# Kernel optimization log

Measured on AMD Instinct MI355X. Metric: run time of the kernel, lower is better.

Reference implementation:

```python
import jax, jax.numpy as jnp
import numpy as np

NUM_HEADS = 16
HIDDEN = 1024
HEAD_DIM = HIDDEN // NUM_HEADS
B, L = 1, 2048


def setup_inputs() -> dict:
    key = jax.random.key(0)
    ks = jax.random.split(key, 5)
    scale = 1.0 / np.sqrt(HIDDEN)
    x = jax.random.normal(ks[0], (B, L, HIDDEN), dtype=jnp.float32)
    Wq = jax.random.normal(ks[1], (HIDDEN, HIDDEN), dtype=jnp.float32) * scale
    Wk = jax.random.normal(ks[2], (HIDDEN, HIDDEN), dtype=jnp.float32) * scale
    Wv = jax.random.normal(ks[3], (HIDDEN, HIDDEN), dtype=jnp.float32) * scale
    Wo = jax.random.normal(ks[4], (HIDDEN, HIDDEN), dtype=jnp.float32) * scale
    return {"x": x, "Wq": Wq, "Wk": Wk, "Wv": Wv, "Wo": Wo}


def reference(x, Wq, Wk, Wv, Wo):
    Bx, Lx, _ = x.shape
    # nn.Linear computes x @ W.T (bias=False)
    q = (x @ Wq.T).reshape(Bx, Lx, NUM_HEADS, HEAD_DIM)
    k = (x @ Wk.T).reshape(Bx, Lx, NUM_HEADS, HEAD_DIM)
    v = (x @ Wv.T).reshape(Bx, Lx, NUM_HEADS, HEAD_DIM)
    # elu(.)+1 feature map
    q = jax.nn.elu(q) + 1.0
    k = jax.nn.elu(k) + 1.0
    # causal linear-attention state via cumsum of kv outer products
    kv = jnp.einsum('blhd,blhe->blhde', k, v)           # [B,L,H,D,D]
    kv_cumsum = jnp.cumsum(kv, axis=1)
    k_cumsum = jnp.cumsum(k, axis=1)
    out = jnp.einsum('blhd,blhde->blhe', q, kv_cumsum)   # [B,L,H,D]
    denom = jnp.clip(jnp.einsum('blhd,blhd->blh', q, k_cumsum), 1e-6, None)
    out = out / denom[..., None]
    return out.reshape(Bx, Lx, HIDDEN) @ Wo.T
```

## Files before the change

kernel.cpp:

```cpp
#include <hip/hip_runtime.h>
#include <hip/hip_bf16.h>

typedef __attribute__((ext_vector_type(8))) short short8;
typedef __attribute__((ext_vector_type(4))) float floatx4;
typedef __attribute__((ext_vector_type(8))) unsigned short ushortx8;
typedef __attribute__((ext_vector_type(4))) unsigned short ushortx4;
typedef unsigned short u16;

#define HIDDEN 1024
#define NH 16
#define HD 64
#define SEQ 2048
#define CHUNK 128
#define NCHUNK (SEQ / CHUNK)

__device__ __forceinline__ u16 f2bf(float f) {
    union { float f; unsigned u; } v; v.f = f;
    unsigned r = v.u + 0x7fffu + ((v.u >> 16) & 1u);
    return (u16)(r >> 16);
}
__device__ __forceinline__ float bf2f(u16 u) {
    union { unsigned u; float f; } v; v.u = ((unsigned)u) << 16;
    return v.f;
}

__device__ __forceinline__ void gl_lds16(const u16* g, u16* l) {
    __builtin_amdgcn_global_load_lds(
        (const __attribute__((address_space(1))) void*)g,
        (__attribute__((address_space(3))) void*)l,
        16, 0, 0);
}

__global__ __launch_bounds__(256)
void convert_all(const float* __restrict__ x,  const float* __restrict__ Wq,
                 const float* __restrict__ Wk, const float* __restrict__ Wv,
                 const float* __restrict__ Wo,
                 u16* __restrict__ xb, u16* __restrict__ Wb, u16* __restrict__ Wob)
{
    const int total4 = 1572864;
    for (int idx = blockIdx.x * 256 + threadIdx.x; idx < total4; idx += gridDim.x * 256) {
        const float4* src; u16* dst; int off;
        if (idx < 524288)       { src = (const float4*)x;  dst = xb;            off = idx; }
        else if (idx < 786432)  { src = (const float4*)Wq; dst = Wb;            off = idx - 524288; }
        else if (idx < 1048576) { src = (const float4*)Wk; dst = Wb + 1048576;  off = idx - 786432; }
        else if (idx < 1310720) { src = (const float4*)Wv; dst = Wb + 2097152;  off = idx - 1048576; }
        else                    { src = (const float4*)Wo; dst = Wob;           off = idx - 1310720; }
        float4 v = src[off];
        ushortx4 u = { f2bf(v.x), f2bf(v.y), f2bf(v.z), f2bf(v.w) };
        *(ushortx4*)(dst + (size_t)off * 4) = u;
    }
}

template<int TM, bool ELU, typename OutT>
__global__ __launch_bounds__(256, 2)
void gemm_m97(const u16* __restrict__ A, const u16* __restrict__ Bm,
              OutT* __restrict__ C, const int K, const int ldc)
{
    constexpr int FI = TM / 32;
    __shared__ u16 As[TM * 64];
    __shared__ u16 Bs[128 * 64];
    const int m0 = blockIdx.y * TM, n0 = blockIdx.x * 128;
    const int t = threadIdx.x;
    const int lane = t & 63, wave = t >> 6;
    const int ln = lane & 15, q4 = lane >> 4;
    const int wm = (wave >> 1) * (TM / 2);
    const int wn = (wave & 1) * 64;
    const int r_in = t >> 3;
    const int csw = (((t & 7) ^ (r_in & 7)) << 3);

    const u16* Ag = A + (size_t)(m0 + r_in) * K + csw;
    const u16* Bg = Bm + (size_t)(n0 + r_in) * K + csw;

    floatx4 acc[FI][4];
#pragma unroll
    for (int i = 0; i < FI; i++)
#pragma unroll
        for (int j = 0; j < 4; j++) acc[i][j] = (floatx4)0.0f;

    for (int k0 = 0; k0 < K; k0 += 64) {
        if (k0) __syncthreads();
#pragma unroll
        for (int i = 0; i < FI; i++)
            gl_lds16(Ag + (size_t)i * 32 * K, &As[i * 2048 + t * 8]);
#pragma unroll
        for (int i = 0; i < 4; i++)
            gl_lds16(Bg + (size_t)i * 32 * K, &Bs[i * 2048 + t * 8]);
        Ag += 64; Bg += 64;
        __syncthreads();
#pragma unroll
        for (int s = 0; s < 2; s++) {
            const int rc = (((s * 4 + q4) ^ (ln & 7)) << 3);
            short8 af[FI], bfr[4];
#pragma unroll
            for (int i = 0; i < FI; i++)
                af[i] = *(const short8*)&As[(wm + i * 16 + ln) * 64 + rc];
#pragma unroll
            for (int j = 0; j < 4; j++)
                bfr[j] = *(const short8*)&Bs[(wn + j * 16 + ln) * 64 + rc];
#pragma unroll
            for (int i = 0; i < FI; i++)
#pragma unroll
                for (int j = 0; j < 4; j++)
                    acc[i][j] = __builtin_amdgcn_mfma_f32_16x16x32_bf16(af[i], bfr[j], acc[i][j], 0, 0, 0);
        }
    }
#pragma unroll
    for (int i = 0; i < FI; i++)
#pragma unroll
        for (int j = 0; j < 4; j++)
#pragma unroll
            for (int rr = 0; rr < 4; rr++) {
                int m = m0 + wm + i * 16 + q4 * 4 + rr;
                int n = n0 + wn + j * 16 + ln;
                float v = acc[i][j][rr];
                if (ELU && n < 2048) v = (v > 0.f) ? (v + 1.f) : __expf(v);
                if constexpr (sizeof(OutT) == 2) C[(size_t)m * ldc + n] = f2bf(v);
                else                             C[(size_t)m * ldc + n] = v;
            }
}

__global__ __launch_bounds__(256, 2)
void chunk_stats(const u16* __restrict__ qkv,
                 float* __restrict__ S_ws, float* __restrict__ ksum_ws)
{
    __shared__ u16 kT[64 * 136];
    __shared__ u16 vT[64 * 136];
    const int c = blockIdx.x, h = blockIdx.y;
    const int t = threadIdx.x;
    const int lane = t & 63, wave = t >> 6;
    const int ln = lane & 15, q4 = lane >> 4;
    {
        const int row = t >> 1, sc = (t & 1) * 32;
        const size_t gk = (size_t)(c * CHUNK + row) * 3072 + 1024 + h * HD + sc;
        u16 kr[32], vr[32];
#pragma unroll
        for (int i = 0; i < 4; i++) {
            *(ushortx8*)&kr[i * 8] = *(const ushortx8*)(qkv + gk + i * 8);
            *(ushortx8*)&vr[i * 8] = *(const ushortx8*)(qkv + gk + 1024 + i * 8);
        }
#pragma unroll
        for (int j = 0; j < 32; j++) {
            kT[(sc + j) * 136 + row] = kr[j];
            vT[(sc + j) * 136 + row] = vr[j];
        }
    }
    __syncthreads();
    floatx4 sacc[4];
#pragma unroll
    for (int j = 0; j < 4; j++) sacc[j] = (floatx4)0.0f;
#pragma unroll
    for (int ks = 0; ks < 4; ks++) {
        short8 af = *(const short8*)&kT[(wave * 16 + ln) * 136 + ks * 32 + q4 * 8];
#pragma unroll
        for (int j = 0; j < 4; j++) {
            short8 bfr = *(const short8*)&vT[(j * 16 + ln) * 136 + ks * 32 + q4 * 8];
            sacc[j] = __builtin_amdgcn_mfma_f32_16x16x32_bf16(af, bfr, sacc[j], 0, 0, 0);
        }
    }
    float* Sp = S_ws + ((size_t)(h * NCHUNK + c) << 12);
#pragma unroll
    for (int j = 0; j < 4; j++)
#pragma unroll
        for (int r = 0; r < 4; r++) {
            int d = wave * 16 + q4 * 4 + r;
            int e = j * 16 + ln;
            Sp[e * 64 + d] = sacc[j][r];
        }
    if (t < 64) {
        float s = 0.f;
#pragma unroll
        for (int j = 0; j < 128; j++) s += bf2f(kT[t * 136 + j]);
        ksum_ws[(h * NCHUNK + c) * 64 + t] = s;
    }
}

__global__ __launch_bounds__(256, 1)
void attn_out(const u16* __restrict__ qkv, const float* __restrict__ S_ws,
              const float* __restrict__ ksum_ws, u16* __restrict__ attnb)
{
    __shared__ __align__(16) u16 smem[32384];
    u16* q_l   = smem;
    u16* k_l   = smem + 9216;
    u16* P_l   = smem;
    u16* vT_l  = smem + 18432;
    u16* kvT_l = smem + 27136;
    float* kpref  = (float*)(smem + 31744);
    float* denom2 = kpref + 64;

    const int c = blockIdx.x, h = blockIdx.y;
    const int t = threadIdx.x;
    const int lane = t & 63, wave = t >> 6;
    const int ln = lane & 15, q4 = lane >> 4;

    {
        const int row = t >> 1, sc = (t & 1) * 32;
        const size_t gq = (size_t)(c * CHUNK + row) * 3072 + h * HD + sc;
#pragma unroll
        for (int i = 0; i < 4; i++) {
            *(ushortx8*)&q_l[row * 72 + sc + i * 8] = *(const ushortx8*)(qkv + gq + i * 8);
            *(ushortx8*)&k_l[row * 72 + sc + i * 8] = *(const ushortx8*)(qkv + gq + 1024 + i * 8);
        }
        u16 vr[32];
#pragma unroll
        for (int i = 0; i < 4; i++) *(ushortx8*)&vr[i * 8] = *(const ushortx8*)(qkv + gq + 2048 + i * 8);
#pragma unroll
        for (int j = 0; j < 32; j++) vT_l[(sc + j) * 136 + row] = vr[j];
    }
    {
        const int e = t >> 2, db = (t & 3) * 16;
        float kv[16];
#pragma unroll
        for (int i = 0; i < 16; i++) kv[i] = 0.f;
        for (int cp = 0; cp < c; cp++) {
            const float* Sp = S_ws + ((size_t)(h * NCHUNK + cp) << 12) + e * 64 + db;
#pragma unroll
            for (int g = 0; g < 4; g++) {
                float4 s4 = *(const float4*)(Sp + g * 4);
                kv[g * 4 + 0] += s4.x; kv[g * 4 + 1] += s4.y;
                kv[g * 4 + 2] += s4.z; kv[g * 4 + 3] += s4.w;
            }
        }
#pragma unroll
        for (int g = 0; g < 4; g++) {
            ushortx4 u = { f2bf(kv[g * 4 + 0]), f2bf(kv[g * 4 + 1]),
                           f2bf(kv[g * 4 + 2]), f2bf(kv[g * 4 + 3]) };
            *(ushortx4*)&kvT_l[e * 72 + db + g * 4] = u;
        }
        if (t < 64) {
            float s = 0.f;
            for (int cp = 0; cp < c; cp++) s += ksum_ws[(h * NCHUNK + cp) * 64 + t];
            kpref[t] = s;
        }
    }
    __syncthreads();

    const int pm = (wave >> 1) * 64, pn = (wave & 1) * 64;
    floatx4 pacc[4][4];
#pragma unroll
    for (int i = 0; i < 4; i++)
#pragma unroll
        for (int j = 0; j < 4; j++) pacc[i][j] = (floatx4)0.0f;
#pragma unroll
    for (int s = 0; s < 2; s++) {
        short8 af[4], bfr[4];
#pragma unroll
        for (int i = 0; i < 4; i++)
            af[i] = *(const short8*)&q_l[(pm + i * 16 + ln) * 72 + s * 32 + q4 * 8];
#pragma unroll
        for (int j = 0; j < 4; j++)
            bfr[j] = *(const short8*)&k_l[(pn + j * 16 + ln) * 72 + s * 32 + q4 * 8];
#pragma unroll
        for (int i = 0; i < 4; i++)
#pragma unroll
            for (int j = 0; j < 4; j++)
                pacc[i][j] = __builtin_amdgcn_mfma_f32_16x16x32_bf16(af[i], bfr[j], pacc[i][j], 0, 0, 0);
    }
#pragma unroll
    for (int i = 0; i < 4; i++)
#pragma unroll
        for (int r = 0; r < 4; r++) {
            int rowi = pm + i * 16 + q4 * 4 + r;
            float rs = 0.f;
#pragma unroll
            for (int j = 0; j < 4; j++) {
                int col = pn + j * 16 + ln;
                float p = pacc[i][j][r];
                if (col > rowi) p = 0.f;
                pacc[i][j][r] = p;
                rs += p;
            }
#pragma unroll
            for (int off = 1; off < 16; off <<= 1) rs += __shfl_xor(rs, off, 64);
            if (ln == 0) denom2[(wave & 1) * 128 + rowi] = rs;
        }
    const int ob = wave * 32;
    floatx4 oacc[2][4];
#pragma unroll
    for (int i = 0; i < 2; i++)
#pragma unroll
        for (int j = 0; j < 4; j++) oacc[i][j] = (floatx4)0.0f;
#pragma unroll
    for (int s = 0; s < 2; s++) {
        short8 af[2], bfr[4];
#pragma unroll
        for (int i2 = 0; i2 < 2; i2++)
            af[i2] = *(const short8*)&q_l[(ob + i2 * 16 + ln) * 72 + s * 32 + q4 * 8];
#pragma unroll
        for (int j = 0; j < 4; j++)
            bfr[j] = *(const short8*)&kvT_l[(j * 16 + ln) * 72 + s * 32 + q4 * 8];
#pragma unroll
        for (int i2 = 0; i2 < 2; i2++)
#pragma unroll
            for (int j = 0; j < 4; j++)
                oacc[i2][j] = __builtin_amdgcn_mfma_f32_16x16x32_bf16(af[i2], bfr[j], oacc[i2][j], 0, 0, 0);
    }
    __syncthreads();
    if (t < 128) {
        float s = 0.f;
#pragma unroll
        for (int d = 0; d < 64; d++) s += bf2f(q_l[t * 72 + d]) * kpref[d];
        denom2[t] += s;
    }
    __syncthreads();
#pragma unroll
    for (int i = 0; i < 4; i++)
#pragma unroll
        for (int j = 0; j < 4; j++)
#pragma unroll
            for (int r = 0; r < 4; r++) {
                int rowi = pm + i * 16 + q4 * 4 + r;
                int col = pn + j * 16 + ln;
                P_l[rowi * 136 + col] = f2bf(pacc[i][j][r]);
            }
    __syncthreads();
    for (int ks = 0; ks <= wave; ks++) {
        short8 af[2], bfr[4];
#pragma unroll
        for (int i2 = 0; i2 < 2; i2++)
            af[i2] = *(const short8*)&P_l[(ob + i2 * 16 + ln) * 136 + ks * 32 + q4 * 8];
#pragma unroll
        for (int j = 0; j < 4; j++)
            bfr[j] = *(const short8*)&vT_l[(j * 16 + ln) * 136 + ks * 32 + q4 * 8];
#pragma unroll
        for (int i2 = 0; i2 < 2; i2++)
#pragma unroll
            for (int j = 0; j < 4; j++)
                oacc[i2][j] = __builtin_amdgcn_mfma_f32_16x16x32_bf16(af[i2], bfr[j], oacc[i2][j], 0, 0, 0);
    }
#pragma unroll
    for (int i2 = 0; i2 < 2; i2++)
#pragma unroll
        for (int j = 0; j < 4; j++)
#pragma unroll
            for (int r = 0; r < 4; r++) {
                int rowi = ob + i2 * 16 + q4 * 4 + r;
                int e = j * 16 + ln;
                float den = denom2[rowi] + denom2[128 + rowi];
                den = fmaxf(den, 1e-6f);
                float val = oacc[i2][j][r] / den;
                attnb[(size_t)(c * CHUNK + rowi) * HIDDEN + h * HD + e] = f2bf(val);
            }
}

extern "C" void kernel_launch(void* const* d_in, const int* in_sizes, int n_in,
                              void* d_out, int out_size, void* d_ws, size_t ws_size,
                              hipStream_t stream)
{
    const float* x  = (const float*)d_in[0];
    const float* Wq = (const float*)d_in[1];
    const float* Wk = (const float*)d_in[2];
    const float* Wv = (const float*)d_in[3];
    const float* Wo = (const float*)d_in[4];
    float* out = (float*)d_out;

    char* ws = (char*)d_ws;
    const size_t MB = 1024 * 1024;
    u16* qkvb  = (u16*)(ws);
    u16* xb    = (u16*)(ws + 12 * MB);
    u16* attnb = (u16*)(ws + 12 * MB);
    u16* Wb    = (u16*)(ws + 16 * MB);
    float* S_ws    = (float*)(ws + 16 * MB);
    float* ksum_ws = (float*)(ws + 20 * MB);
    u16* Wob   = (u16*)(ws + 22 * MB);

    convert_all<<<2048, 256, 0, stream>>>(x, Wq, Wk, Wv, Wo, xb, Wb, Wob);
    gemm_m97<128, true, u16><<<dim3(24, 16), 256, 0, stream>>>(xb, Wb, qkvb, 1024, 3072);
    chunk_stats<<<dim3(NCHUNK, NH), 256, 0, stream>>>(qkvb, S_ws, ksum_ws);
    attn_out<<<dim3(NCHUNK, NH), 256, 0, stream>>>(qkvb, S_ws, ksum_ws, attnb);
    gemm_m97<64, false, float><<<dim3(8, 32), 256, 0, stream>>>(attnb, Wob, out, 1024, 1024);
}
```

Before: 137.5 us.

## Emit transposed K/V from QKV GEMM and shrink GEMM tiles for occupancy

The QKV GEMM epilogue now writes Q/K row-major plus K and V transposed per head, so the chunk_stats and attn_out kernels can load with direct global-to-LDS copies into swizzled layouts. This replaces the scalar LDS transposes. Both GEMMs move to 64-row tiles with more blocks and higher launch bounds to fill more CUs. The cost is extra global writes for the transposed copies and scattered 8-byte stores in the epilogue.

```diff
diff --git a/kernel.cpp b/kernel.cpp
--- a/kernel.cpp
+++ b/kernel.cpp
@@ -51,98 +51,102 @@
     }
 }
 
-template<int TM, bool ELU, typename OutT>
-__global__ __launch_bounds__(256, 2)
-void gemm_m97(const u16* __restrict__ A, const u16* __restrict__ Bm,
-              OutT* __restrict__ C, const int K, const int ldc)
-{
-    constexpr int FI = TM / 32;
-    __shared__ u16 As[TM * 64];
+__global__ __launch_bounds__(256, 3)
+void qkv_gemm64(const u16* __restrict__ A, const u16* __restrict__ Bm,
+                u16* __restrict__ qkb, u16* __restrict__ kT_b, u16* __restrict__ vT_b)
+{
+    __shared__ u16 As[64 * 64];
     __shared__ u16 Bs[128 * 64];
-    const int m0 = blockIdx.y * TM, n0 = blockIdx.x * 128;
+    const int n0 = blockIdx.x * 128, m0 = blockIdx.y * 64;
     const int t = threadIdx.x;
     const int lane = t & 63, wave = t >> 6;
     const int ln = lane & 15, q4 = lane >> 4;
-    const int wm = (wave >> 1) * (TM / 2);
-    const int wn = (wave & 1) * 64;
+    const int wm = (wave >> 1) * 32, wn = (wave & 1) * 64;
     const int r_in = t >> 3;
     const int csw = (((t & 7) ^ (r_in & 7)) << 3);
 
-    const u16* Ag = A + (size_t)(m0 + r_in) * K + csw;
-    const u16* Bg = Bm + (size_t)(n0 + r_in) * K + csw;
-
-    floatx4 acc[FI][4];
-#pragma unroll
-    for (int i = 0; i < FI; i++)
+    const u16* Ag = A + (size_t)(m0 + r_in) * 1024 + csw;
+    const u16* Bg = Bm + (size_t)(n0 + r_in) * 1024 + csw;
+
+    floatx4 acc[2][4];
+#pragma unroll
+    for (int i = 0; i < 2; i++)
 #pragma unroll
         for (int j = 0; j < 4; j++) acc[i][j] = (floatx4)0.0f;
 
-    for (int k0 = 0; k0 < K; k0 += 64) {
+    for (int k0 = 0; k0 < 1024; k0 += 64) {
         if (k0) __syncthreads();
-#pragma unroll
-        for (int i = 0; i < FI; i++)
-            gl_lds16(Ag + (size_t)i * 32 * K, &As[i * 2048 + t * 8]);
+        gl_lds16(Ag, &As[t * 8]);
+        gl_lds16(Ag + 32 * 1024, &As[2048 + t * 8]);
 #pragma unroll
         for (int i = 0; i < 4; i++)
-            gl_lds16(Bg + (size_t)i * 32 * K, &Bs[i * 2048 + t * 8]);
+            gl_lds16(Bg + (size_t)i * 32 * 1024, &Bs[i * 2048 + t * 8]);
         Ag += 64; Bg += 64;
         __syncthreads();
 #pragma unroll
         for (int s = 0; s < 2; s++) {
             const int rc = (((s * 4 + q4) ^ (ln & 7)) << 3);
-            short8 af[FI], bfr[4];
-#pragma unroll
-            for (int i = 0; i < FI; i++)
+            short8 af[2], bfr[4];
+#pragma unroll
+            for (int i = 0; i < 2; i++)
                 af[i] = *(const short8*)&As[(wm + i * 16 + ln) * 64 + rc];
 #pragma unroll
             for (int j = 0; j < 4; j++)
                 bfr[j] = *(const short8*)&Bs[(wn + j * 16 + ln) * 64 + rc];
 #pragma unroll
-            for (int i = 0; i < FI; i++)
+            for (int i = 0; i < 2; i++)
 #pragma unroll
                 for (int j = 0; j < 4; j++)
                     acc[i][j] = __builtin_amdgcn_mfma_f32_16x16x32_bf16(af[i], bfr[j], acc[i][j], 0, 0, 0);
         }
     }
-#pragma unroll
-    for (int i = 0; i < FI; i++)
-#pragma unroll
-        for (int j = 0; j < 4; j++)
-#pragma unroll
-            for (int rr = 0; rr < 4; rr++) {
-                int m = m0 + wm + i * 16 + q4 * 4 + rr;
-                int n = n0 + wn + j * 16 + ln;
-                float v = acc[i][j][rr];
-                if (ELU && n < 2048) v = (v > 0.f) ? (v + 1.f) : __expf(v);
-                if constexpr (sizeof(OutT) == 2) C[(size_t)m * ldc + n] = f2bf(v);
-                else                             C[(size_t)m * ldc + n] = v;
-            }
+    const int grp = n0 >> 10;
+#pragma unroll
+    for (int i = 0; i < 2; i++)
+#pragma unroll
+        for (int j = 0; j < 4; j++) {
+            const int mb = m0 + wm + i * 16 + q4 * 4;
+            const int n = n0 + wn + j * 16 + ln;
+            const int nh = n & 1023, h = nh >> 6, e = nh & 63;
+            float vals[4];
+#pragma unroll
+            for (int r = 0; r < 4; r++) {
+                float v = acc[i][j][r];
+                if (grp < 2) v = (v > 0.f) ? (v + 1.f) : __expf(v);
+                vals[r] = v;
+            }
+            if (grp == 0) {
+#pragma unroll
+                for (int r = 0; r < 4; r++) qkb[(size_t)(mb + r) * 2048 + nh] = f2bf(vals[r]);
+            } else if (grp == 1) {
+#pragma unroll
+                for (int r = 0; r < 4; r++) qkb[(size_t)(mb + r) * 2048 + 1024 + nh] = f2bf(vals[r]);
+                ushortx4 u = { f2bf(vals[0]), f2bf(vals[1]), f2bf(vals[2]), f2bf(vals[3]) };
+                *(ushortx4*)&kT_b[(size_t)(h * 64 + e) * 2048 + mb] = u;
+            } else {
+                ushortx4 u = { f2bf(vals[0]), f2bf(vals[1]), f2bf(vals[2]), f2bf(vals[3]) };
+                *(ushortx4*)&vT_b[(size_t)(h * 64 + e) * 2048 + mb] = u;
+            }
+        }
 }
 
 __global__ __launch_bounds__(256, 2)
-void chunk_stats(const u16* __restrict__ qkv,
-                 float* __restrict__ S_ws, float* __restrict__ ksum_ws)
-{
-    __shared__ u16 kT[64 * 136];
-    __shared__ u16 vT[64 * 136];
+void chunk_stats2(const u16* __restrict__ kT_b, const u16* __restrict__ vT_b,
+                  float* __restrict__ S_ws, float* __restrict__ ksum_ws)
+{
+    __shared__ u16 kT_l[64 * 128];
+    __shared__ u16 vT_l[64 * 128];
     const int c = blockIdx.x, h = blockIdx.y;
     const int t = threadIdx.x;
-    const int lane = t & 63, wave = t >> 6;
+    const int lane = t & 63, w = t >> 6;
     const int ln = lane & 15, q4 = lane >> 4;
-    {
-        const int row = t >> 1, sc = (t & 1) * 32;
-        const size_t gk = (size_t)(c * CHUNK + row) * 3072 + 1024 + h * HD + sc;
-        u16 kr[32], vr[32];
-#pragma unroll
-        for (int i = 0; i < 4; i++) {
-            *(ushortx8*)&kr[i * 8] = *(const ushortx8*)(qkv + gk + i * 8);
-            *(ushortx8*)&vr[i * 8] = *(const ushortx8*)(qkv + gk + 1024 + i * 8);
-        }
-#pragma unroll
-        for (int j = 0; j < 32; j++) {
-            kT[(sc + j) * 136 + row] = kr[j];
-            vT[(sc + j) * 136 + row] = vr[j];
-        }
+#pragma unroll
+    for (int i = 0; i < 4; i++) {
+        const int d0 = w * 16 + i * 4 + (lane >> 4);
+        const int cc = lane & 15;
+        const size_t gsrc = (size_t)(h * 64 + d0) * 2048 + c * 128 + ((cc ^ (d0 & 7)) << 3);
+        gl_lds16(kT_b + gsrc, &kT_l[(w * 16 + i * 4) * 128 + lane * 8]);
+        gl_lds16(vT_b + gsrc, &vT_l[(w * 16 + i * 4) * 128 + lane * 8]);
     }
     __syncthreads();
     floatx4 sacc[4];
@@ -150,10 +154,11 @@
     for (int j = 0; j < 4; j++) sacc[j] = (floatx4)0.0f;
 #pragma unroll
     for (int ks = 0; ks < 4; ks++) {
-        short8 af = *(const short8*)&kT[(wave * 16 + ln) * 136 + ks * 32 + q4 * 8];
+        const int rc = (((ks * 4 + q4) ^ (ln & 7)) << 3);
+        short8 af = *(const short8*)&kT_l[(w * 16 + ln) * 128 + rc];
 #pragma unroll
         for (int j = 0; j < 4; j++) {
-            short8 bfr = *(const short8*)&vT[(j * 16 + ln) * 136 + ks * 32 + q4 * 8];
+            short8 bfr = *(const short8*)&vT_l[(j * 16 + ln) * 128 + rc];
             sacc[j] = __builtin_amdgcn_mfma_f32_16x16x32_bf16(af, bfr, sacc[j], 0, 0, 0);
         }
     }
@@ -162,49 +167,52 @@
     for (int j = 0; j < 4; j++)
 #pragma unroll
         for (int r = 0; r < 4; r++) {
-            int d = wave * 16 + q4 * 4 + r;
+            int d = w * 16 + q4 * 4 + r;
             int e = j * 16 + ln;
             Sp[e * 64 + d] = sacc[j][r];
         }
     if (t < 64) {
         float s = 0.f;
 #pragma unroll
-        for (int j = 0; j < 128; j++) s += bf2f(kT[t * 136 + j]);
+        for (int cc = 0; cc < 16; cc++) {
+            ushortx8 v8 = *(const ushortx8*)&kT_l[t * 128 + cc * 8];
+#pragma unroll
+            for (int jj = 0; jj < 8; jj++) s += bf2f(v8[jj]);
+        }
         ksum_ws[(h * NCHUNK + c) * 64 + t] = s;
     }
 }
 
 __global__ __launch_bounds__(256, 1)
-void attn_out(const u16* __restrict__ qkv, const float* __restrict__ S_ws,
-              const float* __restrict__ ksum_ws, u16* __restrict__ attnb)
-{
-    __shared__ __align__(16) u16 smem[32384];
+void attn_out2(const u16* __restrict__ qkb, const u16* __restrict__ vT_b,
+               const float* __restrict__ S_ws, const float* __restrict__ ksum_ws,
+               u16* __restrict__ attnb)
+{
+    __shared__ __align__(16) u16 smem[29824];
     u16* q_l   = smem;
-    u16* k_l   = smem + 9216;
+    u16* k_l   = smem + 8192;
+    u16* kvT_l = smem + 16384;
     u16* P_l   = smem;
-    u16* vT_l  = smem + 18432;
-    u16* kvT_l = smem + 27136;
-    float* kpref  = (float*)(smem + 31744);
+    u16* vT_l  = smem + 20992;
+    float* kpref  = (float*)(smem + 29184);
     float* denom2 = kpref + 64;
 
     const int c = blockIdx.x, h = blockIdx.y;
     const int t = threadIdx.x;
-    const int lane = t & 63, wave = t >> 6;
+    const int lane = t & 63, w = t >> 6;
     const int ln = lane & 15, q4 = lane >> 4;
 
-    {
-        const int row = t >> 1, sc = (t & 1) * 32;
-        const size_t gq = (size_t)(c * CHUNK + row) * 3072 + h * HD + sc;
-#pragma unroll
-        for (int i = 0; i < 4; i++) {
-            *(ushortx8*)&q_l[row * 72 + sc + i * 8] = *(const ushortx8*)(qkv + gq + i * 8);
-            *(ushortx8*)&k_l[row * 72 + sc + i * 8] = *(const ushortx8*)(qkv + gq + 1024 + i * 8);
-        }
-        u16 vr[32];
-#pragma unroll
-        for (int i = 0; i < 4; i++) *(ushortx8*)&vr[i * 8] = *(const ushortx8*)(qkv + gq + 2048 + i * 8);
-#pragma unroll
-        for (int j = 0; j < 32; j++) vT_l[(sc + j) * 136 + row] = vr[j];
+#pragma unroll
+    for (int i = 0; i < 4; i++) {
+        const int l = i * 32 + w * 8 + (lane >> 3);
+        const int cc = lane & 7;
+        const size_t gq = (size_t)(c * CHUNK + l) * 2048 + h * 64 + ((cc ^ (l & 7)) << 3);
+        gl_lds16(qkb + gq,        &q_l[(i * 32 + w * 8) * 64 + lane * 8]);
+        gl_lds16(qkb + gq + 1024, &k_l[(i * 32 + w * 8) * 64 + lane * 8]);
+        const int d0 = w * 16 + i * 4 + (lane >> 4);
+        const int cv = lane & 15;
+        gl_lds16(vT_b + (size_t)(h * 64 + d0) * 2048 + c * 128 + ((cv ^ (d0 & 7)) << 3),
+                 &vT_l[(w * 16 + i * 4) * 128 + lane * 8]);
     }
     {
         const int e = t >> 2, db = (t & 3) * 16;
@@ -234,7 +242,7 @@
     }
     __syncthreads();
 
-    const int pm = (wave >> 1) * 64, pn = (wave & 1) * 64;
+    const int pm = (w >> 1) * 64, pn = (w & 1) * 64;
     floatx4 pacc[4][4];
 #pragma unroll
     for (int i = 0; i < 4; i++)
@@ -242,13 +250,14 @@
         for (int j = 0; j < 4; j++) pacc[i][j] = (floatx4)0.0f;
 #pragma unroll
     for (int s = 0; s < 2; s++) {
+        const int rc = (((s * 4 + q4) ^ (ln & 7)) << 3);
         short8 af[4], bfr[4];
 #pragma unroll
         for (int i = 0; i < 4; i++)
-            af[i] = *(const short8*)&q_l[(pm + i * 16 + ln) * 72 + s * 32 + q4 * 8];
+            af[i] = *(const short8*)&q_l[(pm + i * 16 + ln) * 64 + rc];
 #pragma unroll
         for (int j = 0; j < 4; j++)
-            bfr[j] = *(const short8*)&k_l[(pn + j * 16 + ln) * 72 + s * 32 + q4 * 8];
+            bfr[j] = *(const short8*)&k_l[(pn + j * 16 + ln) * 64 + rc];
 #pragma unroll
         for (int i = 0; i < 4; i++)
 #pragma unroll
@@ -271,9 +280,9 @@
             }
 #pragma unroll
             for (int off = 1; off < 16; off <<= 1) rs += __shfl_xor(rs, off, 64);
-            if (ln == 0) denom2[(wave & 1) * 128 + rowi] = rs;
-        }
-    const int ob = wave * 32;
+            if (ln == 0) denom2[(w & 1) * 128 + rowi] = rs;
+        }
+    const int ob = w * 32;
     floatx4 oacc[2][4];
 #pragma unroll
     for (int i = 0; i < 2; i++)
@@ -281,10 +290,11 @@
         for (int j = 0; j < 4; j++) oacc[i][j] = (floatx4)0.0f;
 #pragma unroll
     for (int s = 0; s < 2; s++) {
+        const int rc = (((s * 4 + q4) ^ (ln & 7)) << 3);
         short8 af[2], bfr[4];
 #pragma unroll
         for (int i2 = 0; i2 < 2; i2++)
-            af[i2] = *(const short8*)&q_l[(ob + i2 * 16 + ln) * 72 + s * 32 + q4 * 8];
+            af[i2] = *(const short8*)&q_l[(ob + i2 * 16 + ln) * 64 + rc];
 #pragma unroll
         for (int j = 0; j < 4; j++)
             bfr[j] = *(const short8*)&kvT_l[(j * 16 + ln) * 72 + s * 32 + q4 * 8];
@@ -298,7 +308,11 @@
     if (t < 128) {
         float s = 0.f;
 #pragma unroll
-        for (int d = 0; d < 64; d++) s += bf2f(q_l[t * 72 + d]) * kpref[d];
+        for (int c8 = 0; c8 < 8; c8++) {
+            ushortx8 v8 = *(const ushortx8*)&q_l[t * 64 + ((c8 ^ (t & 7)) << 3)];
+#pragma unroll
+            for (int jj = 0; jj < 8; jj++) s += bf2f(v8[jj]) * kpref[c8 * 8 + jj];
+        }
         denom2[t] += s;
     }
     __syncthreads();
@@ -313,14 +327,15 @@
                 P_l[rowi * 136 + col] = f2bf(pacc[i][j][r]);
             }
     __syncthreads();
-    for (int ks = 0; ks <= wave; ks++) {
+    for (int ks = 0; ks <= w; ks++) {
         short8 af[2], bfr[4];
 #pragma unroll
         for (int i2 = 0; i2 < 2; i2++)
             af[i2] = *(const short8*)&P_l[(ob + i2 * 16 + ln) * 136 + ks * 32 + q4 * 8];
+        const int rc = (((ks * 4 + q4) ^ (ln & 7)) << 3);
 #pragma unroll
         for (int j = 0; j < 4; j++)
-            bfr[j] = *(const short8*)&vT_l[(j * 16 + ln) * 136 + ks * 32 + q4 * 8];
+            bfr[j] = *(const short8*)&vT_l[(j * 16 + ln) * 128 + rc];
 #pragma unroll
         for (int i2 = 0; i2 < 2; i2++)
 #pragma unroll
@@ -342,6 +357,66 @@
             }
 }
 
+__global__ __launch_bounds__(256, 3)
+void out_gemm64(const u16* __restrict__ A, const u16* __restrict__ Bm,
+                float* __restrict__ out)
+{
+    __shared__ u16 As[64 * 64];
+    __shared__ u16 Bs[64 * 64];
+    const int n0 = blockIdx.x * 64, m0 = blockIdx.y * 64;
+    const int t = threadIdx.x;
+    const int lane = t & 63, wave = t >> 6;
+    const int ln = lane & 15, q4 = lane >> 4;
+    const int wm = (wave >> 1) * 32, wn = (wave & 1) * 32;
+    const int r_in = t >> 3;
+    const int csw = (((t & 7) ^ (r_in & 7)) << 3);
+
+    const u16* Ag = A + (size_t)(m0 + r_in) * 1024 + csw;
+    const u16* Bg = Bm + (size_t)(n0 + r_in) * 1024 + csw;
+
+    floatx4 acc[2][2];
+#pragma unroll
+    for (int i = 0; i < 2; i++)
+#pragma unroll
+        for (int j = 0; j < 2; j++) acc[i][j] = (floatx4)0.0f;
+
+    for (int k0 = 0; k0 < 1024; k0 += 64) {
+        if (k0) __syncthreads();
+        gl_lds16(Ag, &As[t * 8]);
+        gl_lds16(Ag + 32 * 1024, &As[2048 + t * 8]);
+        gl_lds16(Bg, &Bs[t * 8]);
+        gl_lds16(Bg + 32 * 1024, &Bs[2048 + t * 8]);
+        Ag += 64; Bg += 64;
+        __syncthreads();
+#pragma unroll
+        for (int s = 0; s < 2; s++) {
+            const int rc = (((s * 4 + q4) ^ (ln & 7)) << 3);
+            short8 af[2], bfr[2];
+#pragma unroll
+            for (int i = 0; i < 2; i++)
+                af[i] = *(const short8*)&As[(wm + i * 16 + ln) * 64 + rc];
+#pragma unroll
+            for (int j = 0; j < 2; j++)
+                bfr[j] = *(const short8*)&Bs[(wn + j * 16 + ln) * 64 + rc];
+#pragma unroll
+            for (int i = 0; i < 2; i++)
+#pragma unroll
+                for (int j = 0; j < 2; j++)
+                    acc[i][j] = __builtin_amdgcn_mfma_f32_16x16x32_bf16(af[i], bfr[j], acc[i][j], 0, 0, 0);
+        }
+    }
+#pragma unroll
+    for (int i = 0; i < 2; i++)
+#pragma unroll
+        for (int j = 0; j < 2; j++)
+#pragma unroll
+            for (int r = 0; r < 4; r++) {
+                int m = m0 + wm + i * 16 + q4 * 4 + r;
+                int n = n0 + wn + j * 16 + ln;
+                out[(size_t)m * 1024 + n] = acc[i][j][r];
+            }
+}
+
 extern "C" void kernel_launch(void* const* d_in, const int* in_sizes, int n_in,
                               void* d_out, int out_size, void* d_ws, size_t ws_size,
                               hipStream_t stream)
@@ -355,17 +430,19 @@
 
     char* ws = (char*)d_ws;
     const size_t MB = 1024 * 1024;
-    u16* qkvb  = (u16*)(ws);
-    u16* xb    = (u16*)(ws + 12 * MB);
-    u16* attnb = (u16*)(ws + 12 * MB);
-    u16* Wb    = (u16*)(ws + 16 * MB);
-    float* S_ws    = (float*)(ws + 16 * MB);
-    float* ksum_ws = (float*)(ws + 20 * MB);
-    u16* Wob   = (u16*)(ws + 22 * MB);
+    u16* xb    = (u16*)(ws);
+    u16* Wb    = (u16*)(ws + 4 * MB);
+    u16* Wob   = (u16*)(ws + 10 * MB);
+    u16* qkb   = (u16*)(ws + 12 * MB);
+    u16* kT_b  = (u16*)(ws + 20 * MB);
+    u16* vT_b  = (u16*)(ws + 24 * MB);
+    float* S_ws    = (float*)(ws + 28 * MB);
+    float* ksum_ws = (float*)(ws + 32 * MB);
+    u16* attnb = (u16*)(ws + 33 * MB);
 
     convert_all<<<2048, 256, 0, stream>>>(x, Wq, Wk, Wv, Wo, xb, Wb, Wob);
-    gemm_m97<128, true, u16><<<dim3(24, 16), 256, 0, stream>>>(xb, Wb, qkvb, 1024, 3072);
-    chunk_stats<<<dim3(NCHUNK, NH), 256, 0, stream>>>(qkvb, S_ws, ksum_ws);
-    attn_out<<<dim3(NCHUNK, NH), 256, 0, stream>>>(qkvb, S_ws, ksum_ws, attnb);
-    gemm_m97<64, false, float><<<dim3(8, 32), 256, 0, stream>>>(attnb, Wob, out, 1024, 1024);
-}
+    qkv_gemm64<<<dim3(24, 32), 256, 0, stream>>>(xb, Wb, qkb, kT_b, vT_b);
+    chunk_stats2<<<dim3(NCHUNK, NH), 256, 0, stream>>>(kT_b, vT_b, S_ws, ksum_ws);
+    attn_out2<<<dim3(NCHUNK, NH), 256, 0, stream>>>(qkb, vT_b, S_ws, ksum_ws, attnb);
+    out_gemm64<<<dim3(16, 32), 256, 0, stream>>>(attnb, Wob, out);
+}
```

Result: faster. 130.1 us (-5.4%).
